# Performance work log

Hardware: AMD Instinct MI355X
Metric: run time of the kernel (lower is better)

Reference implementation:

```python
import jax, jax.numpy as jnp
import numpy as np

WINDOW_SIZE = 11
SIGMA = 1.5
MAX_VAL = 1.0
C1 = (0.01 * MAX_VAL) ** 2
C2 = (0.03 * MAX_VAL) ** 2


def _gauss_kernel2d(dtype):
    # gaussian(window_size, sigma) from the torch source: odd window, centered
    x = jnp.arange(WINDOW_SIZE, dtype=jnp.float32) - (WINDOW_SIZE // 2)
    g = jnp.exp(-(x * x) / (2.0 * SIGMA * SIGMA))
    g = g / g.sum()
    return (g[:, None] * g[None, :]).astype(dtype)  # (11, 11), L1-normalized


def _filter2d(x, k2d):
    # reflect-padded depthwise conv, same-size output (matches filter2D)
    c = x.shape[1]
    pad = WINDOW_SIZE // 2
    xp = jnp.pad(x, ((0, 0), (0, 0), (pad, pad), (pad, pad)), mode='reflect')
    kern = jnp.broadcast_to(k2d[None, None], (c, 1, WINDOW_SIZE, WINDOW_SIZE))
    return jax.lax.conv_general_dilated(
        xp, kern, window_strides=(1, 1), padding='VALID',
        dimension_numbers=('NCHW', 'OIHW', 'NCHW'), feature_group_count=c)


def setup_inputs() -> dict:
    key = jax.random.key(0)
    k1, k2 = jax.random.split(key)
    img1 = jax.random.uniform(k1, (16, 3, 512, 512), dtype=jnp.float32)
    img2 = jax.random.uniform(k2, (16, 3, 512, 512), dtype=jnp.float32)
    return {"img1": img1, "img2": img2}


def reference(img1, img2):
    k2d = _gauss_kernel2d(img1.dtype)
    mu1 = _filter2d(img1, k2d)
    mu2 = _filter2d(img2, k2d)
    mu1_sq = mu1 * mu1
    mu2_sq = mu2 * mu2
    mu1_mu2 = mu1 * mu2
    sigma1_sq = _filter2d(img1 * img1, k2d) - mu1_sq
    sigma2_sq = _filter2d(img2 * img2, k2d) - mu2_sq
    sigma12 = _filter2d(img1 * img2, k2d) - mu1_mu2
    ssim_map = ((2.0 * mu1_mu2 + C1) * (2.0 * sigma12 + C2)) / (
        (mu1_sq + mu2_sq + C1) * (sigma1_sq + sigma2_sq + C2))
    # DSSIM loss as in kornia 0.2.x: clamp(1 - ssim, 0, 1) / 2, reduction='none'
    loss = jnp.clip(1.0 - ssim_map, 0.0, 1.0) / 2.0
    return loss
```

## Files before the change

kernel.cpp:

```cpp
#include <hip/hip_runtime.h>

#define IMG_H 512
#define IMG_W 512

__device__ __forceinline__ int reflect512(int t) {
    t = (t < 0) ? -t : t;
    t = (t > 511) ? 1022 - t : t;
    return t;
}

__global__ __launch_bounds__(64, 3) void ssim_kernel(
    const float* __restrict__ img1,
    const float* __restrict__ img2,
    float* __restrict__ out)
{
    const float kW[11] = {
        0.00102838f, 0.00759876f, 0.03600078f, 0.10936055f, 0.21300561f,
        0.26601182f, 0.21300561f, 0.10936055f, 0.03600078f, 0.00759876f,
        0.00102838f };
    const float C1 = 0.0001f;
    const float C2 = 0.0009f;

    const int lane = threadIdx.x;
    const int x0 = blockIdx.x * 64;
    const int y0 = blockIdx.y * 64;
    const size_t pbase = (size_t)blockIdx.z * (IMG_H * IMG_W);
    const float* __restrict__ p1 = img1 + pbase;
    const float* __restrict__ p2 = img2 + pbase;
    float* __restrict__ po = out + pbase;

    __shared__ float2 buf[2][80];

    float r1[11], r2[11], r11[11], r22[11], r12[11];

    const int x = x0 + lane;
    const int gx0 = reflect512(x0 - 5 + lane);
    const int gx1 = reflect512(x0 - 5 + lane + 64);

    for (int sb = 0; sb < 74; sb += 11) {
        #pragma unroll
        for (int r = 0; r < 11; ++r) {
            const int s = sb + r;
            if (s < 74) {
                const int gy = reflect512(y0 - 5 + s);
                const float* row1 = p1 + (size_t)gy * IMG_W;
                const float* row2 = p2 + (size_t)gy * IMG_W;
                float2* b = buf[s & 1];
                b[lane] = make_float2(row1[gx0], row2[gx0]);
                if (lane < 10)
                    b[lane + 64] = make_float2(row1[gx1], row2[gx1]);
                __syncthreads();

                float h1 = 0.f, h2 = 0.f, h11 = 0.f, h22 = 0.f, h12 = 0.f;
                #pragma unroll
                for (int k = 0; k < 11; ++k) {
                    const float2 t = b[lane + k];
                    const float wk = kW[k];
                    const float ta = wk * t.x;
                    const float tb = wk * t.y;
                    h1 += ta;
                    h2 += tb;
                    h11 = fmaf(ta, t.x, h11);
                    h22 = fmaf(tb, t.y, h22);
                    h12 = fmaf(ta, t.y, h12);
                }
                r1[r] = h1; r2[r] = h2; r11[r] = h11; r22[r] = h22; r12[r] = h12;

                if (s >= 10) {
                    float v1 = 0.f, v2 = 0.f, v11 = 0.f, v22 = 0.f, v12 = 0.f;
                    #pragma unroll
                    for (int d = 0; d < 11; ++d) {
                        const int slot = (r + 11 - d) % 11;
                        const float wd = kW[10 - d];
                        v1  = fmaf(wd, r1[slot],  v1);
                        v2  = fmaf(wd, r2[slot],  v2);
                        v11 = fmaf(wd, r11[slot], v11);
                        v22 = fmaf(wd, r22[slot], v22);
                        v12 = fmaf(wd, r12[slot], v12);
                    }
                    const float mu1s = v1 * v1;
                    const float mu2s = v2 * v2;
                    const float mu12 = v1 * v2;
                    const float sg1  = v11 - mu1s;
                    const float sg2  = v22 - mu2s;
                    const float sg12 = v12 - mu12;
                    const float num = fmaf(2.f, mu12, C1) * fmaf(2.f, sg12, C2);
                    const float den = (mu1s + mu2s + C1) * (sg1 + sg2 + C2);
                    float rden = __builtin_amdgcn_rcpf(den);
                    rden = rden * (2.f - den * rden);
                    const float ssim = num * rden;
                    const float loss = 0.5f * fminf(fmaxf(1.f - ssim, 0.f), 1.f);
                    po[(size_t)(y0 + s - 10) * IMG_W + x] = loss;
                }
            }
        }
    }
}

extern "C" void kernel_launch(void* const* d_in, const int* in_sizes, int n_in,
                              void* d_out, int out_size, void* d_ws, size_t ws_size,
                              hipStream_t stream) {
    const float* img1 = (const float*)d_in[0];
    const float* img2 = (const float*)d_in[1];
    float* out = (float*)d_out;
    dim3 grid(IMG_W / 64, IMG_H / 64, 48);
    ssim_kernel<<<grid, dim3(64, 1, 1), 0, stream>>>(img1, img2, out);
}
```

Baseline: 206.3 us.

## Split tiles across two waves, prefetch rows into registers, merge variance accumulators

```diff
diff --git a/kernel.cpp b/kernel.cpp
--- a/kernel.cpp
+++ b/kernel.cpp
@@ -2,6 +2,8 @@
 
 #define IMG_H 512
 #define IMG_W 512
+#define TILE_H 32
+#define ROWS (TILE_H + 10)
 
 __device__ __forceinline__ int reflect512(int t) {
     t = (t < 0) ? -t : t;
@@ -9,7 +11,7 @@
     return t;
 }
 
-__global__ __launch_bounds__(64, 3) void ssim_kernel(
+__global__ __launch_bounds__(128, 6) void ssim_kernel(
     const float* __restrict__ img1,
     const float* __restrict__ img2,
     float* __restrict__ out)
@@ -21,37 +23,62 @@
     const float C1 = 0.0001f;
     const float C2 = 0.0009f;
 
-    const int lane = threadIdx.x;
+    const int tid  = threadIdx.x;
+    const int wv   = tid >> 6;
+    const int lane = tid & 63;
     const int x0 = blockIdx.x * 64;
-    const int y0 = blockIdx.y * 64;
+    const int y0 = blockIdx.y * 64 + wv * TILE_H;
     const size_t pbase = (size_t)blockIdx.z * (IMG_H * IMG_W);
     const float* __restrict__ p1 = img1 + pbase;
     const float* __restrict__ p2 = img2 + pbase;
     float* __restrict__ po = out + pbase;
 
-    __shared__ float2 buf[2][80];
+    __shared__ float2 buf[2][2][80];
+    float2 (* const bufw)[80] = buf[wv];
 
-    float r1[11], r2[11], r11[11], r22[11], r12[11];
+    float ring1[12], ring2[12], ringSS[12], ringAB[12];
+    float pfa[3], pfb[3], pfat[3], pfbt[3];
 
-    const int x = x0 + lane;
+    const int xo  = x0 + lane;
     const int gx0 = reflect512(x0 - 5 + lane);
     const int gx1 = reflect512(x0 - 5 + lane + 64);
 
-    for (int sb = 0; sb < 74; sb += 11) {
+    #pragma unroll
+    for (int p = 0; p < 3; ++p) {
+        const int gy = reflect512(y0 - 5 + p);
+        const float* r1p = p1 + (size_t)gy * IMG_W;
+        const float* r2p = p2 + (size_t)gy * IMG_W;
+        pfa[p] = r1p[gx0];
+        pfb[p] = r2p[gx0];
+        if (lane < 10) { pfat[p] = r1p[gx1]; pfbt[p] = r2p[gx1]; }
+    }
+
+    for (int so = 0; so < 48; so += 12) {
         #pragma unroll
-        for (int r = 0; r < 11; ++r) {
-            const int s = sb + r;
-            if (s < 74) {
-                const int gy = reflect512(y0 - 5 + s);
-                const float* row1 = p1 + (size_t)gy * IMG_W;
-                const float* row2 = p2 + (size_t)gy * IMG_W;
-                float2* b = buf[s & 1];
-                b[lane] = make_float2(row1[gx0], row2[gx0]);
+        for (int r = 0; r < 12; ++r) {
+            const int s = so + r;
+            if (s < ROWS) {
+                const int pi  = r % 3;
+                const int par = r & 1;
+                float2* b = bufw[par];
+
+                b[lane] = make_float2(pfa[pi], pfb[pi]);
                 if (lane < 10)
-                    b[lane + 64] = make_float2(row1[gx1], row2[gx1]);
-                __syncthreads();
+                    b[lane + 64] = make_float2(pfat[pi], pfbt[pi]);
 
-                float h1 = 0.f, h2 = 0.f, h11 = 0.f, h22 = 0.f, h12 = 0.f;
+                if (s + 3 < ROWS) {
+                    const int gy = reflect512(y0 - 5 + s + 3);
+                    const float* r1p = p1 + (size_t)gy * IMG_W;
+                    const float* r2p = p2 + (size_t)gy * IMG_W;
+                    pfa[pi] = r1p[gx0];
+                    pfb[pi] = r2p[gx0];
+                    if (lane < 10) { pfat[pi] = r1p[gx1]; pfbt[pi] = r2p[gx1]; }
+                }
+
+                asm volatile("s_waitcnt lgkmcnt(0)" ::: "memory");
+                __builtin_amdgcn_sched_barrier(0);
+
+                float h1 = 0.f, h2 = 0.f, hss = 0.f, hab = 0.f;
                 #pragma unroll
                 for (int k = 0; k < 11; ++k) {
                     const float2 t = b[lane + k];
@@ -60,37 +87,34 @@
                     const float tb = wk * t.y;
                     h1 += ta;
                     h2 += tb;
-                    h11 = fmaf(ta, t.x, h11);
-                    h22 = fmaf(tb, t.y, h22);
-                    h12 = fmaf(ta, t.y, h12);
+                    hss = fmaf(ta, t.x, hss);
+                    hss = fmaf(tb, t.y, hss);
+                    hab = fmaf(ta, t.y, hab);
                 }
-                r1[r] = h1; r2[r] = h2; r11[r] = h11; r22[r] = h22; r12[r] = h12;
+                ring1[r] = h1; ring2[r] = h2; ringSS[r] = hss; ringAB[r] = hab;
 
                 if (s >= 10) {
-                    float v1 = 0.f, v2 = 0.f, v11 = 0.f, v22 = 0.f, v12 = 0.f;
+                    float v1 = 0.f, v2 = 0.f, vss = 0.f, vab = 0.f;
                     #pragma unroll
                     for (int d = 0; d < 11; ++d) {
-                        const int slot = (r + 11 - d) % 11;
-                        const float wd = kW[10 - d];
-                        v1  = fmaf(wd, r1[slot],  v1);
-                        v2  = fmaf(wd, r2[slot],  v2);
-                        v11 = fmaf(wd, r11[slot], v11);
-                        v22 = fmaf(wd, r22[slot], v22);
-                        v12 = fmaf(wd, r12[slot], v12);
+                        const int slot = (r - d + 12) % 12;
+                        const float wd = kW[d];
+                        v1  = fmaf(wd, ring1[slot],  v1);
+                        v2  = fmaf(wd, ring2[slot],  v2);
+                        vss = fmaf(wd, ringSS[slot], vss);
+                        vab = fmaf(wd, ringAB[slot], vab);
                     }
-                    const float mu1s = v1 * v1;
-                    const float mu2s = v2 * v2;
                     const float mu12 = v1 * v2;
-                    const float sg1  = v11 - mu1s;
-                    const float sg2  = v22 - mu2s;
-                    const float sg12 = v12 - mu12;
+                    const float musq = fmaf(v1, v1, v2 * v2);
+                    const float sgsum = vss - musq;
+                    const float sg12  = vab - mu12;
                     const float num = fmaf(2.f, mu12, C1) * fmaf(2.f, sg12, C2);
-                    const float den = (mu1s + mu2s + C1) * (sg1 + sg2 + C2);
+                    const float den = (musq + C1) * (sgsum + C2);
                     float rden = __builtin_amdgcn_rcpf(den);
                     rden = rden * (2.f - den * rden);
                     const float ssim = num * rden;
                     const float loss = 0.5f * fminf(fmaxf(1.f - ssim, 0.f), 1.f);
-                    po[(size_t)(y0 + s - 10) * IMG_W + x] = loss;
+                    po[(size_t)(y0 + s - 10) * IMG_W + xo] = loss;
                 }
             }
         }
@@ -104,5 +128,5 @@
     const float* img2 = (const float*)d_in[1];
     float* out = (float*)d_out;
     dim3 grid(IMG_W / 64, IMG_H / 64, 48);
-    ssim_kernel<<<grid, dim3(64, 1, 1), 0, stream>>>(img1, img2, out);
+    ssim_kernel<<<grid, dim3(128, 1, 1), 0, stream>>>(img1, img2, out);
 }
```

Result: slower. 561.5 us (+172.2%).
